# Performance work log

Hardware: AMD Instinct MI355X
Metric: run time of the kernel (lower is better)

Reference implementation:

```python
import jax, jax.numpy as jnp
import numpy as np

TEMPERATURE = 0.1
EPS = 1e-12  # matches torch F.normalize default eps


def setup_inputs() -> dict:
    key = jax.random.key(0)
    k1, k2 = jax.random.split(key)
    B, D = 4096, 512
    features1 = jax.random.normal(k1, (B, D), dtype=jnp.float32)
    features2 = jax.random.normal(k2, (B, D), dtype=jnp.float32)
    return {"features1": features1, "features2": features2}


def _l2_normalize(x, axis=1):
    norm = jnp.linalg.norm(x, axis=axis, keepdims=True)
    return x / jnp.maximum(norm, EPS)


def reference(features1, features2):
    B = features1.shape[0]
    f1 = _l2_normalize(features1)
    f2 = _l2_normalize(features2)
    features = jnp.concatenate([f1, f2], axis=0)  # (2B, D)
    sim = jnp.matmul(features, features.T) / TEMPERATURE  # (2B, 2B)
    # mask self-similarity on the diagonal with -inf
    diag = jnp.eye(2 * B, dtype=bool)
    sim = jnp.where(diag, -jnp.inf, sim)
    # positive pair labels: row i pairs with i+B (first half) / i-B (second half)
    labels = jnp.concatenate([jnp.arange(B) + B, jnp.arange(B)], axis=0)
    log_probs = jax.nn.log_softmax(sim, axis=-1)  # (2B, 2B)
    nll = -jnp.take_along_axis(log_probs, labels[:, None], axis=1)[:, 0]
    return jnp.mean(nll)
```

## Files before the change

kernel.cpp:

```cpp
#include <hip/hip_runtime.h>

#define NROWS 8192
#define HALF_N 4096
#define DIM 512
#define INV_T 10.0f
#define NRB 64
#define NBLOCKS 2080

typedef __attribute__((ext_vector_type(4))) float f32x4;
typedef __attribute__((ext_vector_type(2))) long long2v;

__device__ __forceinline__ void async16(const void* g, void* l) {
  __builtin_amdgcn_global_load_lds(
      (const __attribute__((address_space(1))) unsigned int*)g,
      (__attribute__((address_space(3))) unsigned int*)l, 16, 0, 0);
}

__global__ __launch_bounds__(256) void norm_cast_k(
    const float* __restrict__ f1, const float* __restrict__ f2,
    unsigned char* __restrict__ Fa, unsigned char* __restrict__ Fb,
    float* __restrict__ rowsum, float* __restrict__ out) {
  int wave = threadIdx.x >> 6;
  int lane = threadIdx.x & 63;
  int row = blockIdx.x * 4 + wave;
  const float* src = (row < HALF_N) ? (f1 + (size_t)row * DIM)
                                    : (f2 + (size_t)(row - HALF_N) * DIM);
  const float4* p = reinterpret_cast<const float4*>(src + lane * 8);
  float4 v0 = p[0];
  float4 v1 = p[1];
  float ss = v0.x*v0.x + v0.y*v0.y + v0.z*v0.z + v0.w*v0.w
           + v1.x*v1.x + v1.y*v1.y + v1.z*v1.z + v1.w*v1.w;
  #pragma unroll
  for (int off = 1; off < 64; off <<= 1) ss += __shfl_xor(ss, off);
  float scale = 1.0f / fmaxf(sqrtf(ss), 1e-12f);
  int lo = __builtin_amdgcn_cvt_pk_fp8_f32(v0.x * scale, v0.y * scale, 0, false);
  lo = __builtin_amdgcn_cvt_pk_fp8_f32(v0.z * scale, v0.w * scale, lo, true);
  int hi = __builtin_amdgcn_cvt_pk_fp8_f32(v1.x * scale, v1.y * scale, 0, false);
  hi = __builtin_amdgcn_cvt_pk_fp8_f32(v1.z * scale, v1.w * scale, hi, true);
  int2 val = make_int2(lo, hi);
  int u = lane & 7;
  int g = lane >> 3;
  int pos = 2 * (u & 3) + (u >> 2);
  *reinterpret_cast<int2*>(Fb + (size_t)row * DIM + g * 64 + pos * 8) = val;
  int chunk = g * 4 + (u & 3);
  int slot = u >> 2;
  *reinterpret_cast<int2*>(Fa + (size_t)(row >> 4) * 8192 + chunk * 256 +
                           (row & 15) * 16 + slot * 8) = val;
  if (lane == 0) rowsum[row] = 0.0f;
  if (blockIdx.x == 0 && threadIdx.x == 0) out[0] = 0.0f;
}

__global__ __launch_bounds__(256, 3) void sym_gemm_k(
    const unsigned char* __restrict__ Fa, const unsigned char* __restrict__ Fb,
    float* __restrict__ rowsum, float* __restrict__ pairsim) {
  int bx = blockIdx.x;
  int gbx = (bx & 7) * (NBLOCKS / 8) + (bx >> 3);
  int rb = 0, rem = gbx;
  while (rem >= NRB - rb) { rem -= NRB - rb; ++rb; }
  const int cb = rb + rem;
  const int row0 = rb * 128, col0 = cb * 128;

  const int tid = threadIdx.x;
  const int wave = tid >> 6;
  const int lane = tid & 63;
  const int quad = lane >> 4;
  const int colid = lane & 15;
  const int wr0 = (wave >> 1) * 64;
  const int wc0 = (wave & 1) * 64;

  __shared__ __align__(16) unsigned char Blds[128 * 64];
  __shared__ float redrow[128];
  __shared__ float redcol[128];

  if (tid < 128) { redrow[tid] = 0.0f; redcol[tid] = 0.0f; }

  const unsigned char* srcB[2]; unsigned char* dstB[2];
  #pragma unroll
  for (int seg = 0; seg < 2; ++seg) {
    int inst = wave + seg * 4;
    int r = inst * 16 + (lane >> 2);
    int c = (lane & 3) ^ ((r >> 1) & 3);
    srcB[seg] = Fb + (size_t)(col0 + r) * DIM + c * 16;
    dstB[seg] = Blds + inst * 1024;
  }

  const unsigned char* agp[4];
  #pragma unroll
  for (int t = 0; t < 4; ++t)
    agp[t] = Fa + (size_t)((row0 + wr0 + t * 16) >> 4) * 8192 +
             quad * 256 + colid * 16;

  const unsigned char* bfp[4];
  #pragma unroll
  for (int t = 0; t < 4; ++t) {
    int rc = wc0 + t * 16 + colid;
    bfp[t] = Blds + rc * 64 + ((quad ^ ((rc >> 1) & 3)) << 4);
  }

  f32x4 acc[4][4];
  #pragma unroll
  for (int t = 0; t < 4; ++t)
    #pragma unroll
    for (int u = 0; u < 4; ++u) acc[t][u] = (f32x4){0.f, 0.f, 0.f, 0.f};

  for (int kc = 0; kc < 8; ++kc) {
    __syncthreads();
    const size_t ko = (size_t)kc * 64;
    #pragma unroll
    for (int seg = 0; seg < 2; ++seg)
      async16(srcB[seg] + ko, dstB[seg]);
    long2v af[4];
    #pragma unroll
    for (int t = 0; t < 4; ++t)
      af[t] = *reinterpret_cast<const long2v*>(agp[t] + kc * 1024);
    __syncthreads();

    long2v bf[4];
    #pragma unroll
    for (int u = 0; u < 4; ++u) bf[u] = *reinterpret_cast<const long2v*>(bfp[u]);
    #pragma unroll
    for (int s = 0; s < 2; ++s)
      #pragma unroll
      for (int t = 0; t < 4; ++t)
        #pragma unroll
        for (int u = 0; u < 4; ++u)
          acc[t][u] = __builtin_amdgcn_mfma_f32_16x16x32_fp8_fp8(
              af[t][s], bf[u][s], acc[t][u], 0, 0, 0);
  }

  float re[4][4];
  float ce[4];
  #pragma unroll
  for (int t = 0; t < 4; ++t)
    #pragma unroll
    for (int r = 0; r < 4; ++r) re[t][r] = 0.0f;
  #pragma unroll
  for (int u = 0; u < 4; ++u) ce[u] = 0.0f;

  #pragma unroll
  for (int t = 0; t < 4; ++t) {
    #pragma unroll
    for (int u = 0; u < 4; ++u) {
      f32x4 a = acc[t][u];
      const int gc = col0 + wc0 + u * 16 + colid;
      #pragma unroll
      for (int r = 0; r < 4; ++r) {
        int grow = row0 + wr0 + t * 16 + quad * 4 + r;
        float sim = a[r] * INV_T;
        float e = (gc > grow) ? __expf(sim) : 0.0f;
        re[t][r] += e;
        ce[u] += e;
        if (gc == grow + HALF_N && grow < HALF_N) {
          pairsim[grow] = sim;
          pairsim[gc] = sim;
        }
      }
    }
  }

  #pragma unroll
  for (int t = 0; t < 4; ++t)
    #pragma unroll
    for (int r = 0; r < 4; ++r) {
      float v = re[t][r];
      v += __shfl_xor(v, 1); v += __shfl_xor(v, 2);
      v += __shfl_xor(v, 4); v += __shfl_xor(v, 8);
      if (colid == 0) atomicAdd(&redrow[wr0 + t * 16 + quad * 4 + r], v);
    }
  #pragma unroll
  for (int u = 0; u < 4; ++u) {
    float v = ce[u];
    v += __shfl_xor(v, 16); v += __shfl_xor(v, 32);
    if (lane < 16) atomicAdd(&redcol[wc0 + u * 16 + colid], v);
  }
  __syncthreads();
  if (tid < 128) atomicAdd(&rowsum[row0 + tid], redrow[tid]);
  else           atomicAdd(&rowsum[col0 + tid - 128], redcol[tid - 128]);
}

__global__ __launch_bounds__(256) void finalize_k(
    const float* __restrict__ rowsum, const float* __restrict__ pairsim,
    float* __restrict__ out) {
  int i = blockIdx.x * 256 + threadIdx.x;
  float local = logf(rowsum[i]) - pairsim[i];
  #pragma unroll
  for (int off = 1; off < 64; off <<= 1) local += __shfl_xor(local, off);
  if ((threadIdx.x & 63) == 0)
    atomicAdd(out, local * (1.0f / (float)NROWS));
}

extern "C" void kernel_launch(void* const* d_in, const int* in_sizes, int n_in,
                              void* d_out, int out_size, void* d_ws, size_t ws_size,
                              hipStream_t stream) {
  const float* f1 = (const float*)d_in[0];
  const float* f2 = (const float*)d_in[1];
  unsigned char* Fa = (unsigned char*)d_ws;
  unsigned char* Fb = Fa + (size_t)NROWS * DIM;
  float* rowsum = (float*)(Fb + (size_t)NROWS * DIM);
  float* pairsim = rowsum + NROWS;
  float* out = (float*)d_out;

  norm_cast_k<<<NROWS / 4, 256, 0, stream>>>(f1, f2, Fa, Fb, rowsum, out);
  sym_gemm_k<<<NBLOCKS, 256, 0, stream>>>(Fa, Fb, rowsum, pairsim);
  finalize_k<<<NROWS / 256, 256, 0, stream>>>(rowsum, pairsim, out);
}
```

Baseline: 104.8 us.

## Switch FP8 GEMM to 16x16x128 scaled MFMA with K=128 tiles

Replaces the 16x16x32 fp8 MFMA with the gfx950 16x16x128 f8f6f4 scaled MFMA, using unit E8M0 scales. The K chunk per iteration doubles to 128, halving loop trips and barriers. The global and LDS layouts of the A and B operands change to match, with a new XOR swizzle on B in LDS. This cuts MFMA issue count and sync overhead, but uses twice the LDS, which may lower occupancy, and the new layout mapping has to agree exactly with the operand order the instruction expects.

```diff
diff --git a/kernel.cpp b/kernel.cpp
--- a/kernel.cpp
+++ b/kernel.cpp
@@ -8,7 +8,10 @@
 #define NBLOCKS 2080
 
 typedef __attribute__((ext_vector_type(4))) float f32x4;
-typedef __attribute__((ext_vector_type(2))) long long2v;
+typedef __attribute__((ext_vector_type(4))) int i32x4;
+typedef __attribute__((ext_vector_type(8))) int i32x8;
+
+#define SCALE_ONE 0x7F7F7F7F
 
 __device__ __forceinline__ void async16(const void* g, void* l) {
   __builtin_amdgcn_global_load_lds(
@@ -38,14 +41,10 @@
   int hi = __builtin_amdgcn_cvt_pk_fp8_f32(v1.x * scale, v1.y * scale, 0, false);
   hi = __builtin_amdgcn_cvt_pk_fp8_f32(v1.z * scale, v1.w * scale, hi, true);
   int2 val = make_int2(lo, hi);
-  int u = lane & 7;
-  int g = lane >> 3;
-  int pos = 2 * (u & 3) + (u >> 2);
-  *reinterpret_cast<int2*>(Fb + (size_t)row * DIM + g * 64 + pos * 8) = val;
-  int chunk = g * 4 + (u & 3);
-  int slot = u >> 2;
-  *reinterpret_cast<int2*>(Fa + (size_t)(row >> 4) * 8192 + chunk * 256 +
-                           (row & 15) * 16 + slot * 8) = val;
+  *reinterpret_cast<int2*>(Fb + (size_t)row * DIM + lane * 8) = val;
+  *reinterpret_cast<int2*>(Fa + (size_t)(row >> 4) * 8192 + (lane >> 2) * 512 +
+                           ((lane >> 1) & 1) * 256 + (row & 15) * 16 +
+                           (lane & 1) * 8) = val;
   if (lane == 0) rowsum[row] = 0.0f;
   if (blockIdx.x == 0 && threadIdx.x == 0) out[0] = 0.0f;
 }
@@ -68,33 +67,35 @@
   const int wr0 = (wave >> 1) * 64;
   const int wc0 = (wave & 1) * 64;
 
-  __shared__ __align__(16) unsigned char Blds[128 * 64];
+  __shared__ __align__(16) unsigned char Blds[128 * 128];
   __shared__ float redrow[128];
   __shared__ float redcol[128];
 
   if (tid < 128) { redrow[tid] = 0.0f; redcol[tid] = 0.0f; }
 
-  const unsigned char* srcB[2]; unsigned char* dstB[2];
-  #pragma unroll
-  for (int seg = 0; seg < 2; ++seg) {
-    int inst = wave + seg * 4;
-    int r = inst * 16 + (lane >> 2);
-    int c = (lane & 3) ^ ((r >> 1) & 3);
-    srcB[seg] = Fb + (size_t)(col0 + r) * DIM + c * 16;
-    dstB[seg] = Blds + inst * 1024;
+  const unsigned char* srcB[4]; unsigned char* dstB[4];
+  {
+    int rr = lane >> 3;
+    int lc = (lane & 7) ^ rr;
+    #pragma unroll
+    for (int seg = 0; seg < 4; ++seg) {
+      int inst = wave * 4 + seg;
+      srcB[seg] = Fb + (size_t)(col0 + inst * 8 + rr) * DIM + lc * 16;
+      dstB[seg] = Blds + inst * 1024;
+    }
   }
 
   const unsigned char* agp[4];
   #pragma unroll
   for (int t = 0; t < 4; ++t)
     agp[t] = Fa + (size_t)((row0 + wr0 + t * 16) >> 4) * 8192 +
-             quad * 256 + colid * 16;
-
-  const unsigned char* bfp[4];
-  #pragma unroll
-  for (int t = 0; t < 4; ++t) {
-    int rc = wc0 + t * 16 + colid;
-    bfp[t] = Blds + rc * 64 + ((quad ^ ((rc >> 1) & 3)) << 4);
+             quad * 512 + colid * 16;
+
+  int boff[4];
+  #pragma unroll
+  for (int u = 0; u < 4; ++u) {
+    int rc = wc0 + u * 16 + colid;
+    boff[u] = rc * 128 + (((2 * quad) ^ (rc & 7)) << 4);
   }
 
   f32x4 acc[4][4];
@@ -103,29 +104,34 @@
     #pragma unroll
     for (int u = 0; u < 4; ++u) acc[t][u] = (f32x4){0.f, 0.f, 0.f, 0.f};
 
-  for (int kc = 0; kc < 8; ++kc) {
+  for (int kc = 0; kc < 4; ++kc) {
     __syncthreads();
-    const size_t ko = (size_t)kc * 64;
-    #pragma unroll
-    for (int seg = 0; seg < 2; ++seg)
-      async16(srcB[seg] + ko, dstB[seg]);
-    long2v af[4];
+    #pragma unroll
+    for (int seg = 0; seg < 4; ++seg)
+      async16(srcB[seg] + kc * 128, dstB[seg]);
+    union { i32x4 h[2]; i32x8 v; } af[4];
+    #pragma unroll
+    for (int t = 0; t < 4; ++t) {
+      const unsigned char* ap = agp[t] + kc * 2048;
+      af[t].h[0] = *reinterpret_cast<const i32x4*>(ap);
+      af[t].h[1] = *reinterpret_cast<const i32x4*>(ap + 256);
+    }
+    __syncthreads();
+
+    union { i32x4 h[2]; i32x8 v; } bf[4];
+    #pragma unroll
+    for (int u = 0; u < 4; ++u) {
+      bf[u].h[0] = *reinterpret_cast<const i32x4*>(Blds + boff[u]);
+      bf[u].h[1] = *reinterpret_cast<const i32x4*>(Blds + (boff[u] ^ 16));
+    }
     #pragma unroll
     for (int t = 0; t < 4; ++t)
-      af[t] = *reinterpret_cast<const long2v*>(agp[t] + kc * 1024);
-    __syncthreads();
-
-    long2v bf[4];
-    #pragma unroll
-    for (int u = 0; u < 4; ++u) bf[u] = *reinterpret_cast<const long2v*>(bfp[u]);
-    #pragma unroll
-    for (int s = 0; s < 2; ++s)
       #pragma unroll
-      for (int t = 0; t < 4; ++t)
-        #pragma unroll
-        for (int u = 0; u < 4; ++u)
-          acc[t][u] = __builtin_amdgcn_mfma_f32_16x16x32_fp8_fp8(
-              af[t][s], bf[u][s], acc[t][u], 0, 0, 0);
+      for (int u = 0; u < 4; ++u)
+        acc[t][u] = __builtin_amdgcn_mfma_scale_f32_16x16x128_f8f6f4(
+            af[t].v, bf[u].v, acc[t][u],
+            0 , 0 ,
+            0, SCALE_ONE, 0, SCALE_ONE);
   }
 
   float re[4][4];
```

Result: slower. 260.3 us (+148.3%).

## Double-buffer B tile in LDS and prefetch next A fragments

Applied to the files above, without the earlier changes.

Adds a second LDS buffer for the B tile so the async global-to-LDS load for the next K chunk is issued before the MFMAs on the current chunk, and prefetches the next A register fragments the same way. This drops one barrier per iteration and aims to hide global load latency behind the MFMAs. It doubles B LDS usage and raises register pressure from the extra A fragments, which could lower occupancy under the launch-bounds hint of 3 blocks per CU. The single barrier per iteration relies on the hardware wait for the async LDS loads, which may not be guaranteed to complete before the next iteration reads the buffer.

```diff
diff --git a/kernel.cpp b/kernel.cpp
--- a/kernel.cpp
+++ b/kernel.cpp
@@ -68,20 +68,20 @@
   const int wr0 = (wave >> 1) * 64;
   const int wc0 = (wave & 1) * 64;
 
-  __shared__ __align__(16) unsigned char Blds[128 * 64];
+  __shared__ __align__(16) unsigned char Blds[2][128 * 64];
   __shared__ float redrow[128];
   __shared__ float redcol[128];
 
   if (tid < 128) { redrow[tid] = 0.0f; redcol[tid] = 0.0f; }
 
-  const unsigned char* srcB[2]; unsigned char* dstB[2];
+  const unsigned char* srcB[2]; int dstO[2];
   #pragma unroll
   for (int seg = 0; seg < 2; ++seg) {
     int inst = wave + seg * 4;
     int r = inst * 16 + (lane >> 2);
     int c = (lane & 3) ^ ((r >> 1) & 3);
     srcB[seg] = Fb + (size_t)(col0 + r) * DIM + c * 16;
-    dstB[seg] = Blds + inst * 1024;
+    dstO[seg] = inst * 1024;
   }
 
   const unsigned char* agp[4];
@@ -90,11 +90,11 @@
     agp[t] = Fa + (size_t)((row0 + wr0 + t * 16) >> 4) * 8192 +
              quad * 256 + colid * 16;
 
-  const unsigned char* bfp[4];
+  int boff[4];
   #pragma unroll
   for (int t = 0; t < 4; ++t) {
     int rc = wc0 + t * 16 + colid;
-    bfp[t] = Blds + rc * 64 + ((quad ^ ((rc >> 1) & 3)) << 4);
+    boff[t] = rc * 64 + ((quad ^ ((rc >> 1) & 3)) << 4);
   }
 
   f32x4 acc[4][4];
@@ -103,21 +103,34 @@
     #pragma unroll
     for (int u = 0; u < 4; ++u) acc[t][u] = (f32x4){0.f, 0.f, 0.f, 0.f};
 
+  #pragma unroll
+  for (int seg = 0; seg < 2; ++seg)
+    async16(srcB[seg], &Blds[0][0] + dstO[seg]);
+  long2v afc[4];
+  #pragma unroll
+  for (int t = 0; t < 4; ++t)
+    afc[t] = *reinterpret_cast<const long2v*>(agp[t]);
+  __syncthreads();
+
+  #pragma unroll
   for (int kc = 0; kc < 8; ++kc) {
-    __syncthreads();
-    const size_t ko = (size_t)kc * 64;
-    #pragma unroll
-    for (int seg = 0; seg < 2; ++seg)
-      async16(srcB[seg] + ko, dstB[seg]);
-    long2v af[4];
-    #pragma unroll
-    for (int t = 0; t < 4; ++t)
-      af[t] = *reinterpret_cast<const long2v*>(agp[t] + kc * 1024);
-    __syncthreads();
+    const int cur = kc & 1;
+    if (kc < 7) {
+      #pragma unroll
+      for (int seg = 0; seg < 2; ++seg)
+        async16(srcB[seg] + (kc + 1) * 64, &Blds[cur ^ 1][0] + dstO[seg]);
+    }
+    long2v afn[4];
+    if (kc < 7) {
+      #pragma unroll
+      for (int t = 0; t < 4; ++t)
+        afn[t] = *reinterpret_cast<const long2v*>(agp[t] + (kc + 1) * 1024);
+    }
 
     long2v bf[4];
     #pragma unroll
-    for (int u = 0; u < 4; ++u) bf[u] = *reinterpret_cast<const long2v*>(bfp[u]);
+    for (int u = 0; u < 4; ++u)
+      bf[u] = *reinterpret_cast<const long2v*>(&Blds[cur][0] + boff[u]);
     #pragma unroll
     for (int s = 0; s < 2; ++s)
       #pragma unroll
@@ -125,7 +138,13 @@
         #pragma unroll
         for (int u = 0; u < 4; ++u)
           acc[t][u] = __builtin_amdgcn_mfma_f32_16x16x32_fp8_fp8(
-              af[t][s], bf[u][s], acc[t][u], 0, 0, 0);
+              afc[t][s], bf[u][s], acc[t][u], 0, 0, 0);
+
+    __syncthreads();
+    if (kc < 7) {
+      #pragma unroll
+      for (int t = 0; t < 4; ++t) afc[t] = afn[t];
+    }
   }
 
   float re[4][4];
```

Measured after the change: 108.6 us. 3.6% more time.

## Stage both GEMM operands through a 4-deep async LDS ring and drop Fa

Applied to the files above, without the earlier changes.

The GEMM now loads both A and B tiles with async global-to-LDS copies into a 4-stage ring buffer, using vmcnt waits so loads overlap MFMA work, instead of reading A straight from global into registers and syncing twice per K-step. The separate pre-tiled Fa copy is removed, so the norm kernel writes only one fp8 layout. It also raises MFMA wave priority. The cost is 64KB of LDS per block and launch bounds lowered from 3 to 2 blocks per CU, which reduces occupancy.

```diff
diff --git a/kernel.cpp b/kernel.cpp
--- a/kernel.cpp
+++ b/kernel.cpp
@@ -18,8 +18,8 @@
 
 __global__ __launch_bounds__(256) void norm_cast_k(
     const float* __restrict__ f1, const float* __restrict__ f2,
-    unsigned char* __restrict__ Fa, unsigned char* __restrict__ Fb,
-    float* __restrict__ rowsum, float* __restrict__ out) {
+    unsigned char* __restrict__ Fb, float* __restrict__ rowsum,
+    float* __restrict__ out) {
   int wave = threadIdx.x >> 6;
   int lane = threadIdx.x & 63;
   int row = blockIdx.x * 4 + wave;
@@ -42,16 +42,12 @@
   int g = lane >> 3;
   int pos = 2 * (u & 3) + (u >> 2);
   *reinterpret_cast<int2*>(Fb + (size_t)row * DIM + g * 64 + pos * 8) = val;
-  int chunk = g * 4 + (u & 3);
-  int slot = u >> 2;
-  *reinterpret_cast<int2*>(Fa + (size_t)(row >> 4) * 8192 + chunk * 256 +
-                           (row & 15) * 16 + slot * 8) = val;
   if (lane == 0) rowsum[row] = 0.0f;
   if (blockIdx.x == 0 && threadIdx.x == 0) out[0] = 0.0f;
 }
 
-__global__ __launch_bounds__(256, 3) void sym_gemm_k(
-    const unsigned char* __restrict__ Fa, const unsigned char* __restrict__ Fb,
+__global__ __launch_bounds__(256, 2) void sym_gemm_k(
+    const unsigned char* __restrict__ Fb,
     float* __restrict__ rowsum, float* __restrict__ pairsim) {
   int bx = blockIdx.x;
   int gbx = (bx & 7) * (NBLOCKS / 8) + (bx >> 3);
@@ -68,65 +64,88 @@
   const int wr0 = (wave >> 1) * 64;
   const int wc0 = (wave & 1) * 64;
 
-  __shared__ __align__(16) unsigned char Blds[128 * 64];
-  __shared__ float redrow[128];
-  __shared__ float redcol[128];
-
-  if (tid < 128) { redrow[tid] = 0.0f; redcol[tid] = 0.0f; }
-
-  const unsigned char* srcB[2]; unsigned char* dstB[2];
-  #pragma unroll
-  for (int seg = 0; seg < 2; ++seg) {
-    int inst = wave + seg * 4;
-    int r = inst * 16 + (lane >> 2);
-    int c = (lane & 3) ^ ((r >> 1) & 3);
-    srcB[seg] = Fb + (size_t)(col0 + r) * DIM + c * 16;
-    dstB[seg] = Blds + inst * 1024;
+  __shared__ __align__(16) unsigned char smem[65536];
+
+  const int rloc = lane >> 2;
+  const int lch = (lane & 3) ^ ((rloc >> 1) & 3);
+  const unsigned char* srcA0 = Fb + (size_t)(row0 + wave * 16 + rloc) * DIM + lch * 16;
+  const unsigned char* srcA1 = Fb + (size_t)(row0 + (wave + 4) * 16 + rloc) * DIM + lch * 16;
+  const unsigned char* srcB0 = Fb + (size_t)(col0 + wave * 16 + rloc) * DIM + lch * 16;
+  const unsigned char* srcB1 = Fb + (size_t)(col0 + (wave + 4) * 16 + rloc) * DIM + lch * 16;
+  const int d0 = wave * 1024, d1 = (wave + 4) * 1024;
+
+  int aoff[4], boff[4];
+  #pragma unroll
+  for (int t = 0; t < 4; ++t) {
+    int ra = wr0 + t * 16 + colid;
+    aoff[t] = ra * 64 + ((quad ^ ((ra >> 1) & 3)) << 4);
+    int rc = wc0 + t * 16 + colid;
+    boff[t] = rc * 64 + ((quad ^ ((rc >> 1) & 3)) << 4);
   }
 
-  const unsigned char* agp[4];
+  f32x4 acc[4][4];
   #pragma unroll
   for (int t = 0; t < 4; ++t)
-    agp[t] = Fa + (size_t)((row0 + wr0 + t * 16) >> 4) * 8192 +
-             quad * 256 + colid * 16;
-
-  const unsigned char* bfp[4];
-  #pragma unroll
-  for (int t = 0; t < 4; ++t) {
-    int rc = wc0 + t * 16 + colid;
-    bfp[t] = Blds + rc * 64 + ((quad ^ ((rc >> 1) & 3)) << 4);
-  }
-
-  f32x4 acc[4][4];
-  #pragma unroll
-  for (int t = 0; t < 4; ++t)
     #pragma unroll
     for (int u = 0; u < 4; ++u) acc[t][u] = (f32x4){0.f, 0.f, 0.f, 0.f};
 
-  for (int kc = 0; kc < 8; ++kc) {
-    __syncthreads();
-    const size_t ko = (size_t)kc * 64;
-    #pragma unroll
-    for (int seg = 0; seg < 2; ++seg)
-      async16(srcB[seg] + ko, dstB[seg]);
-    long2v af[4];
-    #pragma unroll
-    for (int t = 0; t < 4; ++t)
-      af[t] = *reinterpret_cast<const long2v*>(agp[t] + kc * 1024);
-    __syncthreads();
-
-    long2v bf[4];
-    #pragma unroll
-    for (int u = 0; u < 4; ++u) bf[u] = *reinterpret_cast<const long2v*>(bfp[u]);
-    #pragma unroll
-    for (int s = 0; s < 2; ++s)
-      #pragma unroll
-      for (int t = 0; t < 4; ++t)
-        #pragma unroll
-        for (int u = 0; u < 4; ++u)
-          acc[t][u] = __builtin_amdgcn_mfma_f32_16x16x32_fp8_fp8(
-              af[t][s], bf[u][s], acc[t][u], 0, 0, 0);
-  }
+#define STAGE_ROUND(KC) { \
+    unsigned char* As_ = smem + ((KC) & 3) * 8192; \
+    unsigned char* Bs_ = smem + 32768 + ((KC) & 3) * 8192; \
+    async16(srcA0 + (KC) * 64, As_ + d0); \
+    async16(srcA1 + (KC) * 64, As_ + d1); \
+    async16(srcB0 + (KC) * 64, Bs_ + d0); \
+    async16(srcB1 + (KC) * 64, Bs_ + d1); \
+    __builtin_amdgcn_sched_barrier(0); }
+
+#define COMPUTE_ROUND(KC, VN) { \
+    asm volatile("s_waitcnt vmcnt(" VN ")" ::: "memory"); \
+    __builtin_amdgcn_s_barrier(); \
+    __builtin_amdgcn_sched_barrier(0); \
+    const unsigned char* Ab_ = smem + ((KC) & 3) * 8192; \
+    const unsigned char* Bb_ = smem + 32768 + ((KC) & 3) * 8192; \
+    long2v af[4], bf[4]; \
+    _Pragma("unroll") \
+    for (int t = 0; t < 4; ++t) \
+      af[t] = *reinterpret_cast<const long2v*>(Ab_ + aoff[t]); \
+    _Pragma("unroll") \
+    for (int u = 0; u < 4; ++u) \
+      bf[u] = *reinterpret_cast<const long2v*>(Bb_ + boff[u]); \
+    __builtin_amdgcn_s_setprio(1); \
+    _Pragma("unroll") \
+    for (int s = 0; s < 2; ++s) \
+      _Pragma("unroll") \
+      for (int t = 0; t < 4; ++t) \
+        _Pragma("unroll") \
+        for (int u = 0; u < 4; ++u) \
+          acc[t][u] = __builtin_amdgcn_mfma_f32_16x16x32_fp8_fp8( \
+              af[t][s], bf[u][s], acc[t][u], 0, 0, 0); \
+    __builtin_amdgcn_s_setprio(0); }
+
+  STAGE_ROUND(0) STAGE_ROUND(1) STAGE_ROUND(2) STAGE_ROUND(3)
+
+  COMPUTE_ROUND(0, "12")
+  __builtin_amdgcn_s_barrier(); STAGE_ROUND(4)
+  COMPUTE_ROUND(1, "12")
+  __builtin_amdgcn_s_barrier(); STAGE_ROUND(5)
+  COMPUTE_ROUND(2, "12")
+  __builtin_amdgcn_s_barrier(); STAGE_ROUND(6)
+  COMPUTE_ROUND(3, "12")
+  __builtin_amdgcn_s_barrier(); STAGE_ROUND(7)
+  COMPUTE_ROUND(4, "12")
+  COMPUTE_ROUND(5, "8")
+  COMPUTE_ROUND(6, "4")
+  COMPUTE_ROUND(7, "0")
+
+#undef STAGE_ROUND
+#undef COMPUTE_ROUND
+
+  __syncthreads();
+  float* redrow = reinterpret_cast<float*>(smem);
+  float* redcol = reinterpret_cast<float*>(smem) + 128;
+  if (tid < 128) redrow[tid] = 0.0f;
+  else           redcol[tid - 128] = 0.0f;
+  __syncthreads();
 
   float re[4][4];
   float ce[4];
@@ -194,13 +213,12 @@
                               hipStream_t stream) {
   const float* f1 = (const float*)d_in[0];
   const float* f2 = (const float*)d_in[1];
-  unsigned char* Fa = (unsigned char*)d_ws;
-  unsigned char* Fb = Fa + (size_t)NROWS * DIM;
+  unsigned char* Fb = (unsigned char*)d_ws;
   float* rowsum = (float*)(Fb + (size_t)NROWS * DIM);
   float* pairsim = rowsum + NROWS;
   float* out = (float*)d_out;
 
-  norm_cast_k<<<NROWS / 4, 256, 0, stream>>>(f1, f2, Fa, Fb, rowsum, out);
-  sym_gemm_k<<<NBLOCKS, 256, 0, stream>>>(Fa, Fb, rowsum, pairsim);
+  norm_cast_k<<<NROWS / 4, 256, 0, stream>>>(f1, f2, Fb, rowsum, out);
+  sym_gemm_k<<<NBLOCKS, 256, 0, stream>>>(Fb, rowsum, pairsim);
   finalize_k<<<NROWS / 256, 256, 0, stream>>>(rowsum, pairsim, out);
 }
```

After: 118.0 us. 12.5% more time.
